# Kernel optimization log

Hardware: AMD Instinct MI355X
Metric: run time of the kernel (lower is better)

## Reference

```python
import jax, jax.numpy as jnp
import numpy as np

EMB = 1024
HEADS = 16
B, T = 4, 2048


def setup_inputs() -> dict:
    key = jax.random.key(0)
    ks = jax.random.split(key, 9)
    s = 1.0 / np.sqrt(EMB)
    return {
        "x": jax.random.normal(ks[0], (B, T, EMB), dtype=jnp.float32),
        "Wq": jax.random.normal(ks[1], (EMB, EMB), dtype=jnp.float32) * s,
        "bq": jnp.zeros((EMB,), dtype=jnp.float32),
        "Wk": jax.random.normal(ks[2], (EMB, EMB), dtype=jnp.float32) * s,
        "bk": jnp.zeros((EMB,), dtype=jnp.float32),
        "Wv": jax.random.normal(ks[3], (EMB, EMB), dtype=jnp.float32) * s,
        "bv": jnp.zeros((EMB,), dtype=jnp.float32),
        "Wo": jax.random.normal(ks[4], (EMB, EMB), dtype=jnp.float32) * s,
        "bo": jnp.zeros((EMB,), dtype=jnp.float32),
    }


def reference(x, Wq, bq, Wk, bk, Wv, bv, Wo, bo):
    b, t, e = x.shape
    h = HEADS
    hd = e // h
    scale = 1.0 / np.sqrt(hd).astype(np.float32)

    q = (x @ Wq + bq).reshape(b, t, h, hd).transpose(0, 2, 1, 3)  # [b,h,t,hd]
    k = (x @ Wk + bk).reshape(b, t, h, hd).transpose(0, 2, 1, 3)
    v = (x @ Wv + bv).reshape(b, t, h, hd).transpose(0, 2, 1, 3)

    scores = jnp.einsum('bhqd,bhkd->bhqk', q, k) * scale  # [b,h,t,t]
    causal = jnp.tril(jnp.ones((t, t), dtype=bool))  # strict upper triangle masked
    scores = jnp.where(causal, scores, -jnp.inf)
    attn = jax.nn.softmax(scores, axis=-1)
    out = jnp.einsum('bhqk,bhkd->bhqd', attn, v)  # [b,h,t,hd]
    out = out.transpose(0, 2, 1, 3).reshape(b, t, e)
    return out @ Wo + bo
```

## Files before the change

kernel.cpp:

```cpp
#include <hip/hip_runtime.h>
#include <hip/hip_bf16.h>

#define TT   2048
#define NB   4
#define EMB_ 1024
#define NH   16
#define HD   64

typedef __bf16 bf16x8 __attribute__((ext_vector_type(8)));
typedef float  f32x4  __attribute__((ext_vector_type(4)));
typedef short  short4v __attribute__((ext_vector_type(4)));

__device__ inline short f2bf(float f) {
  unsigned u = __builtin_bit_cast(unsigned, f);
  u += 0x7fffu + ((u >> 16) & 1u);
  return (short)(u >> 16);
}

__device__ __forceinline__ unsigned pk2bf(float a, float b) {
  unsigned ua = __builtin_bit_cast(unsigned, a);
  unsigned ub = __builtin_bit_cast(unsigned, b);
  ua += 0x7fffu + ((ua >> 16) & 1u);
  ub += 0x7fffu + ((ub >> 16) & 1u);
  return __builtin_amdgcn_perm(ub, ua, 0x07060302u);
}

__device__ __forceinline__ void gl_lds16(const short* g, short* l) {
  __builtin_amdgcn_global_load_lds(
      (const __attribute__((address_space(1))) unsigned int*)g,
      (__attribute__((address_space(3))) unsigned int*)l, 16, 0, 0);
}

__global__ void convert_w(const float* __restrict__ Wq, const float* __restrict__ Wk,
                          const float* __restrict__ Wv, const float* __restrict__ Wo,
                          short* __restrict__ Wt) {
  __shared__ short tile[32][33];
  const float* W = (blockIdx.z == 0) ? Wq : (blockIdx.z == 1) ? Wk
                   : (blockIdx.z == 2) ? Wv : Wo;
  short* out = Wt + (size_t)blockIdx.z * EMB_ * EMB_;
  int k0 = blockIdx.x * 32, n0 = blockIdx.y * 32;
  int t = threadIdx.x;
  int r = t >> 3, c4 = (t & 7) * 4;
  f32x4 v = *(const f32x4*)&W[(size_t)(k0 + r) * EMB_ + n0 + c4];
#pragma unroll
  for (int j = 0; j < 4; j++) tile[r][c4 + j] = f2bf(v[j]);
  __syncthreads();
  short4v w;
#pragma unroll
  for (int j = 0; j < 4; j++) w[j] = tile[c4 + j][r];
  *(short4v*)&out[(size_t)(n0 + r) * EMB_ + k0 + c4] = w;
}

__global__ void convert_x(const float* __restrict__ x, short* __restrict__ xb) {
  size_t i = ((size_t)blockIdx.x * 256 + threadIdx.x) * 8;
  f32x4 a = *(const f32x4*)&x[i];
  f32x4 b = *(const f32x4*)&x[i + 4];
  short t[8];
#pragma unroll
  for (int j = 0; j < 4; j++) { t[j] = f2bf(a[j]); t[4 + j] = f2bf(b[j]); }
  *(bf16x8*)&xb[i] = *(const bf16x8*)t;
}

__global__ __launch_bounds__(512, 2)
void gemm8(const short* __restrict__ A, const short* __restrict__ W,
           const float* __restrict__ b0, const float* __restrict__ b1,
           const float* __restrict__ b2,
           void* O0, void* O1, void* O2, int vmode_z, int o32, int scale_z) {
  __shared__ __align__(16) short S[65536];
  const int tid = threadIdx.x;
  const int wave = tid >> 6, lane = tid & 63;
  const int lg = lane >> 4, lc = lane & 15;
  const int wm = (wave >> 2) * 128, wn = (wave & 3) * 64;
  const int m0 = blockIdx.x * 256;
  const int n0g = blockIdx.y * 256;
  const int z = n0g >> 10;
  const float* bias = (z == 0) ? b0 : (z == 1) ? b1 : b2;
  void* Out = (z == 0) ? O0 : (z == 1) ? O1 : O2;
  const bool vmode = (z == vmode_z);
  const float osc = (z == scale_z) ? 0.125f : 1.0f;

  const int srow = lane >> 3;
  const int scol = ((lane & 7) ^ srow) * 8;
  const int g0 = ((0 * 4 + lg) ^ (lc & 7)) * 8;
  const int g1 = ((1 * 4 + lg) ^ (lc & 7)) * 8;

  f32x4 acc[8][4];
#pragma unroll
  for (int i = 0; i < 8; i++)
#pragma unroll
    for (int j = 0; j < 4; j++) acc[i][j] = (f32x4)0.0f;

  auto stA = [&](int buf, int half, int kt) {
    const int kk = kt * 64;
#pragma unroll
    for (int c = 0; c < 2; c++) {
      const int rl = half * 128 + c * 64 + wave * 8;
      gl_lds16(&A[(size_t)(m0 + rl + srow) * EMB_ + kk + scol],
               S + buf * 16384 + rl * 64);
    }
  };
  auto stB = [&](int buf, int half, int kt) {
    const int kk = kt * 64;
#pragma unroll
    for (int c = 0; c < 2; c++) {
      const int rl = half * 128 + c * 64 + wave * 8;
      gl_lds16(&W[(size_t)(n0g + rl + srow) * EMB_ + kk + scol],
               S + 32768 + buf * 16384 + rl * 64);
    }
  };

  stA(0, 0, 0); stA(0, 1, 0); stB(0, 0, 0); stB(0, 1, 0);
  stA(1, 0, 1); stA(1, 1, 1); stB(1, 0, 1); stB(1, 1, 1);
  asm volatile("s_waitcnt vmcnt(8)" ::: "memory");
  __builtin_amdgcn_sched_barrier(0);
  __builtin_amdgcn_s_barrier();

  const int NT = EMB_ / 64;
  bf16x8 af[4][2], bN01[2][2], bN23[2][2];

#pragma unroll 1
  for (int kt = 0; kt < NT; kt++) {
    const int cur = kt & 1, nxt = cur ^ 1;
    const short* Ac = S + cur * 16384;
    const short* Bc = S + 32768 + cur * 16384;

#pragma unroll
    for (int mi = 0; mi < 4; mi++) {
      af[mi][0] = *(const bf16x8*)&Ac[(wm + mi * 16 + lc) * 64 + g0];
      af[mi][1] = *(const bf16x8*)&Ac[(wm + mi * 16 + lc) * 64 + g1];
    }
#pragma unroll
    for (int ni = 0; ni < 2; ni++) {
      bN01[ni][0] = *(const bf16x8*)&Bc[(wn + ni * 16 + lc) * 64 + g0];
      bN01[ni][1] = *(const bf16x8*)&Bc[(wn + ni * 16 + lc) * 64 + g1];
    }
    if (kt > 0 && kt + 1 < NT) stA(nxt, 0, kt + 1);
    __builtin_amdgcn_s_barrier();
    asm volatile("s_waitcnt lgkmcnt(0)" ::: "memory");
    __builtin_amdgcn_sched_barrier(0);
    __builtin_amdgcn_s_setprio(1);
#pragma unroll
    for (int mi = 0; mi < 4; mi++)
#pragma unroll
      for (int ni = 0; ni < 2; ni++) {
        acc[mi][ni] = __builtin_amdgcn_mfma_f32_16x16x32_bf16(af[mi][0], bN01[ni][0], acc[mi][ni], 0, 0, 0);
        acc[mi][ni] = __builtin_amdgcn_mfma_f32_16x16x32_bf16(af[mi][1], bN01[ni][1], acc[mi][ni], 0, 0, 0);
      }
    __builtin_amdgcn_s_setprio(0);
    __builtin_amdgcn_s_barrier();

#pragma unroll
    for (int ni = 0; ni < 2; ni++) {
      bN23[ni][0] = *(const bf16x8*)&Bc[(wn + (ni + 2) * 16 + lc) * 64 + g0];
      bN23[ni][1] = *(const bf16x8*)&Bc[(wn + (ni + 2) * 16 + lc) * 64 + g1];
    }
    if (kt > 0 && kt + 1 < NT) stA(nxt, 1, kt + 1);
    __builtin_amdgcn_s_barrier();
    asm volatile("s_waitcnt lgkmcnt(0)" ::: "memory");
    __builtin_amdgcn_sched_barrier(0);
    __builtin_amdgcn_s_setprio(1);
#pragma unroll
    for (int mi = 0; mi < 4; mi++)
#pragma unroll
      for (int ni = 0; ni < 2; ni++) {
        acc[mi][ni + 2] = __builtin_amdgcn_mfma_f32_16x16x32_bf16(af[mi][0], bN23[ni][0], acc[mi][ni + 2], 0, 0, 0);
        acc[mi][ni + 2] = __builtin_amdgcn_mfma_f32_16x16x32_bf16(af[mi][1], bN23[ni][1], acc[mi][ni + 2], 0, 0, 0);
      }
    __builtin_amdgcn_s_setprio(0);
    __builtin_amdgcn_s_barrier();

#pragma unroll
    for (int mi = 0; mi < 4; mi++) {
      af[mi][0] = *(const bf16x8*)&Ac[(wm + (mi + 4) * 16 + lc) * 64 + g0];
      af[mi][1] = *(const bf16x8*)&Ac[(wm + (mi + 4) * 16 + lc) * 64 + g1];
    }
    if (kt + 2 < NT) stB(cur, 0, kt + 2);
    __builtin_amdgcn_s_barrier();
    asm volatile("s_waitcnt lgkmcnt(0)" ::: "memory");
    __builtin_amdgcn_sched_barrier(0);
    __builtin_amdgcn_s_setprio(1);
#pragma unroll
    for (int mi = 0; mi < 4; mi++)
#pragma unroll
      for (int ni = 0; ni < 2; ni++) {
        acc[mi + 4][ni] = __builtin_amdgcn_mfma_f32_16x16x32_bf16(af[mi][0], bN01[ni][0], acc[mi + 4][ni], 0, 0, 0);
        acc[mi + 4][ni] = __builtin_amdgcn_mfma_f32_16x16x32_bf16(af[mi][1], bN01[ni][1], acc[mi + 4][ni], 0, 0, 0);
      }
    __builtin_amdgcn_s_setprio(0);
    __builtin_amdgcn_s_barrier();

    if (kt + 2 < NT) stB(cur, 1, kt + 2);
    __builtin_amdgcn_s_barrier();
    __builtin_amdgcn_s_setprio(1);
#pragma unroll
    for (int mi = 0; mi < 4; mi++)
#pragma unroll
      for (int ni = 0; ni < 2; ni++) {
        acc[mi + 4][ni + 2] = __builtin_amdgcn_mfma_f32_16x16x32_bf16(af[mi][0], bN23[ni][0], acc[mi + 4][ni + 2], 0, 0, 0);
        acc[mi + 4][ni + 2] = __builtin_amdgcn_mfma_f32_16x16x32_bf16(af[mi][1], bN23[ni][1], acc[mi + 4][ni + 2], 0, 0, 0);
      }
    __builtin_amdgcn_s_setprio(0);
    if (kt == NT - 2) {
      asm volatile("s_waitcnt vmcnt(0)" ::: "memory");
    } else if (kt < NT - 2) {
      asm volatile("s_waitcnt vmcnt(4)" ::: "memory");
    }
    __builtin_amdgcn_sched_barrier(0);
    __builtin_amdgcn_s_barrier();
  }

#pragma unroll
  for (int ni = 0; ni < 4; ni++) {
    int colg = n0g + wn + ni * 16 + lc;
    int col = colg & (EMB_ - 1);
    float bv = bias[col];
#pragma unroll
    for (int mi = 0; mi < 8; mi++) {
#pragma unroll
      for (int r = 0; r < 4; r++) {
        int row = m0 + wm + mi * 16 + lg * 4 + r;
        float v = (acc[mi][ni][r] + bv) * osc;
        if (vmode) {
          int b = row >> 11, t = row & (TT - 1);
          int h = col >> 6, d = col & (HD - 1);
          ((short*)Out)[((size_t)((b * NH + h) * HD + d)) * TT + t] = f2bf(v);
        } else if (o32) {
          ((float*)Out)[(size_t)row * EMB_ + col] = v;
        } else {
          ((short*)Out)[(size_t)row * EMB_ + col] = f2bf(v);
        }
      }
    }
  }
}

__global__ __launch_bounds__(256, 4)
void gemm_bt(const void* __restrict__ A, int a32,
             const short* __restrict__ WtBase,
             const float* __restrict__ b0, const float* __restrict__ b1,
             const float* __restrict__ b2,
             void* O0, void* O1, void* O2, int vmode_z, int o32, int scale_z) {
  __shared__ __align__(16) short As[128 * 72];
  __shared__ __align__(16) short Bs[128 * 72];
  const int tid = threadIdx.x;
  const int z = blockIdx.z;
  const short* W    = WtBase + (size_t)z * EMB_ * EMB_;
  const float* bias = (z == 0) ? b0 : (z == 1) ? b1 : b2;
  void* Out         = (z == 0) ? O0 : (z == 1) ? O1 : O2;
  const bool vmode = (z == vmode_z);
  const float osc = (z == scale_z) ? 0.125f : 1.0f;

  const int m0 = blockIdx.x * 128;
  const int n0 = blockIdx.y * 128;
  const int wave = tid >> 6, lane = tid & 63;
  const int wm = (wave >> 1) * 64, wn = (wave & 1) * 64;
  const int lg = lane >> 4, lc = lane & 15;

  f32x4 acc[4][4];
#pragma unroll
  for (int i = 0; i < 4; i++)
#pragma unroll
    for (int j = 0; j < 4; j++) acc[i][j] = (f32x4)0.0f;

  for (int kk = 0; kk < EMB_; kk += 64) {
    __syncthreads();
#pragma unroll
    for (int i = 0; i < 4; i++) {
      int s = i * 256 + tid;
      int row = s >> 3, c = s & 7;
      size_t base = (size_t)(m0 + row) * EMB_ + kk + c * 8;
      bf16x8 av;
      if (a32) {
        const float* Af = (const float*)A + base;
        f32x4 u0 = *(const f32x4*)Af;
        f32x4 u1 = *(const f32x4*)(Af + 4);
        short tmp[8];
#pragma unroll
        for (int j = 0; j < 4; j++) { tmp[j] = f2bf(u0[j]); tmp[4 + j] = f2bf(u1[j]); }
        av = *(const bf16x8*)tmp;
      } else {
        av = *(const bf16x8*)((const short*)A + base);
      }
      *(bf16x8*)&As[row * 72 + c * 8] = av;
    }
#pragma unroll
    for (int i = 0; i < 4; i++) {
      int s = i * 256 + tid;
      int row = s >> 3, c = s & 7;
      *(bf16x8*)&Bs[row * 72 + c * 8] =
          *(const bf16x8*)&W[(size_t)(n0 + row) * EMB_ + kk + c * 8];
    }
    __syncthreads();
#pragma unroll
    for (int ks = 0; ks < 2; ks++) {
      bf16x8 af[4], bfr[4];
#pragma unroll
      for (int mi = 0; mi < 4; mi++)
        af[mi] = *(const bf16x8*)&As[(wm + mi * 16 + lc) * 72 + ks * 32 + lg * 8];
#pragma unroll
      for (int ni = 0; ni < 4; ni++)
        bfr[ni] = *(const bf16x8*)&Bs[(wn + ni * 16 + lc) * 72 + ks * 32 + lg * 8];
#pragma unroll
      for (int mi = 0; mi < 4; mi++)
#pragma unroll
        for (int ni = 0; ni < 4; ni++)
          acc[mi][ni] = __builtin_amdgcn_mfma_f32_16x16x32_bf16(af[mi], bfr[ni], acc[mi][ni], 0, 0, 0);
    }
  }

#pragma unroll
  for (int ni = 0; ni < 4; ni++) {
    int col = n0 + wn + ni * 16 + lc;
    float bv = bias[col];
#pragma unroll
    for (int mi = 0; mi < 4; mi++) {
#pragma unroll
      for (int r = 0; r < 4; r++) {
        int row = m0 + wm + mi * 16 + lg * 4 + r;
        float v = (acc[mi][ni][r] + bv) * osc;
        if (vmode) {
          int b = row >> 11, t = row & (TT - 1);
          int h = col >> 6, d = col & (HD - 1);
          ((short*)Out)[((size_t)((b * NH + h) * HD + d)) * TT + t] = f2bf(v);
        } else if (o32) {
          ((float*)Out)[(size_t)row * EMB_ + col] = v;
        } else {
          ((short*)Out)[(size_t)row * EMB_ + col] = f2bf(v);
        }
      }
    }
  }
}

__global__ __launch_bounds__(256, 2)
void attn_fwd(const short* Q, const short* K, const short* Vt, short* O) {
  __shared__ __align__(16) short Ks[128 * 72];
  __shared__ __align__(16) short Vs[64 * 136];
  __shared__ __align__(16) short Ps[4][16 * 72];
  const int tid = threadIdx.x;
  const int bh = blockIdx.y;
  const int b = bh >> 4, h = bh & (NH - 1);
  const int qtA = 15 - (int)blockIdx.x;
  const int qtB = (int)blockIdx.x;
  const int wave = tid >> 6, lane = tid & 63;
  const int lg = lane >> 4, lc = lane & 15;

  bf16x8 qf[2][2][2];
#pragma unroll
  for (int pt = 0; pt < 2; pt++) {
    const int qt = pt ? qtB : qtA;
#pragma unroll
    for (int rb = 0; rb < 2; rb++) {
      const int qrow = b * TT + qt * 128 + rb * 64 + wave * 16 + lc;
      qf[pt][rb][0] = *(const bf16x8*)&Q[(size_t)qrow * EMB_ + h * HD + lg * 8];
      qf[pt][rb][1] = *(const bf16x8*)&Q[(size_t)qrow * EMB_ + h * HD + 32 + lg * 8];
    }
  }

  f32x4 o[2][2][4];
#pragma unroll
  for (int pt = 0; pt < 2; pt++)
#pragma unroll
    for (int rb = 0; rb < 2; rb++)
#pragma unroll
      for (int ni = 0; ni < 4; ni++) o[pt][rb][ni] = (f32x4)0.0f;
  float lsum[2][2] = {{0.f, 0.f}, {0.f, 0.f}};

  bf16x8 kreg[4], vreg[4];

  auto issue_loads = [&](int ktt) {
    const int kb = ktt * 128;
#pragma unroll
    for (int i = 0; i < 4; i++) {
      int s = i * 256 + tid;
      kreg[i] = *(const bf16x8*)&K[(size_t)(b * TT + kb + (s >> 3)) * EMB_ + h * HD + (s & 7) * 8];
      vreg[i] = *(const bf16x8*)&Vt[(size_t)(bh * HD + (s >> 4)) * TT + kb + (s & 15) * 8];
    }
  };
  auto write_lds = [&]() {
#pragma unroll
    for (int i = 0; i < 4; i++) {
      int s = i * 256 + tid;
      *(bf16x8*)&Ks[(s >> 3) * 72 + (s & 7) * 8] = kreg[i];
      *(bf16x8*)&Vs[(s >> 4) * 136 + (s & 15) * 8] = vreg[i];
    }
  };

  auto compute_tile = [&](int qt, bf16x8 (&qft)[2][2], f32x4 (&ot)[2][4],
                          float (&ls)[2], int ktt) {
    const int q0 = qt * 128;
#pragma unroll
    for (int chunk = 0; chunk < 2; chunk++) {
      const int cg = 2 * ktt + chunk;
#pragma unroll
      for (int rb = 0; rb < 2; rb++) {
        const int qbase = q0 + rb * 64 + wave * 16;
        if (cg * 64 > qbase + 15) continue;
        const bool diag = (cg == 2 * qt + rb);
        const int qg = qbase + lc;

        f32x4 s4[4];
#pragma unroll
        for (int ni = 0; ni < 4; ni++) s4[ni] = (f32x4)0.0f;
#pragma unroll
        for (int ks = 0; ks < 2; ks++) {
          bf16x8 kf[4];
#pragma unroll
          for (int ni = 0; ni < 4; ni++)
            kf[ni] = *(const bf16x8*)&Ks[(chunk * 64 + ni * 16 + lc) * 72 + ks * 32 + lg * 8];
#pragma unroll
          for (int ni = 0; ni < 4; ni++)
            s4[ni] = __builtin_amdgcn_mfma_f32_16x16x32_bf16(kf[ni], qft[rb][ks], s4[ni], 0, 0, 0);
        }

#pragma unroll
        for (int ni = 0; ni < 4; ni++) {
          float p[4];
#pragma unroll
          for (int r = 0; r < 4; r++) {
            float v = s4[ni][r];
            if (diag) {
              int keyg = cg * 64 + ni * 16 + lg * 4 + r;
              if (keyg > qg) v = -1e30f;
            }
            p[r] = __expf(v - 6.0f);
            ls[rb] += p[r];
          }
          uint2 dd;
          dd.x = pk2bf(p[0], p[1]);
          dd.y = pk2bf(p[2], p[3]);
          *(uint2*)&Ps[wave][lc * 72 + ni * 16 + lg * 4] = dd;
        }

#pragma unroll
        for (int ks2 = 0; ks2 < 2; ks2++) {
          bf16x8 pa = *(const bf16x8*)&Ps[wave][lc * 72 + ks2 * 32 + lg * 8];
          bf16x8 vf[4];
#pragma unroll
          for (int ni = 0; ni < 4; ni++)
            vf[ni] = *(const bf16x8*)&Vs[(ni * 16 + lc) * 136 + chunk * 64 + ks2 * 32 + lg * 8];
#pragma unroll
          for (int ni = 0; ni < 4; ni++)
            ot[rb][ni] = __builtin_amdgcn_mfma_f32_16x16x32_bf16(pa, vf[ni], ot[rb][ni], 0, 0, 0);
        }
      }
    }
  };

  const int ntiles = qtA + 1;

  issue_loads(0);
  for (int ktt = 0; ktt < ntiles; ktt++) {
    __syncthreads();
    write_lds();
    if (ktt + 1 < ntiles) issue_loads(ktt + 1);
    __syncthreads();

    compute_tile(qtA, qf[0], o[0], lsum[0], ktt);
    if (ktt <= qtB)
      compute_tile(qtB, qf[1], o[1], lsum[1], ktt);
  }

#pragma unroll
  for (int pt = 0; pt < 2; pt++) {
    const int qt = pt ? qtB : qtA;
    const int q0 = qt * 128;
    float linv[2][4];
#pragma unroll
    for (int rb = 0; rb < 2; rb++) {
      float red = lsum[pt][rb];
      red += __shfl_xor(red, 16, 64);
      red += __shfl_xor(red, 32, 64);
#pragma unroll
      for (int r = 0; r < 4; r++)
        linv[rb][r] = 1.0f / __shfl(red, lg * 4 + r, 64);
    }
#pragma unroll
    for (int rb = 0; rb < 2; rb++) {
#pragma unroll
      for (int ni = 0; ni < 4; ni++) {
#pragma unroll
        for (int r = 0; r < 4; r++) {
          int token = b * TT + q0 + rb * 64 + wave * 16 + lg * 4 + r;
          int col = h * HD + ni * 16 + lc;
          O[(size_t)token * EMB_ + col] = f2bf(o[pt][rb][ni][r] * linv[rb][r]);
        }
      }
    }
  }
}

extern "C" void kernel_launch(void* const* d_in, const int* in_sizes, int n_in,
                              void* d_out, int out_size, void* d_ws, size_t ws_size,
                              hipStream_t stream) {
  const float* x  = (const float*)d_in[0];
  const float* Wq = (const float*)d_in[1];
  const float* bq = (const float*)d_in[2];
  const float* Wk = (const float*)d_in[3];
  const float* bk = (const float*)d_in[4];
  const float* Wv = (const float*)d_in[5];
  const float* bv = (const float*)d_in[6];
  const float* Wo = (const float*)d_in[7];
  const float* bo = (const float*)d_in[8];

  short* Wt = (short*)d_ws;
  short* Qb = Wt + (size_t)4 * EMB_ * EMB_;

  convert_w<<<dim3(32, 32, 4), 256, 0, stream>>>(Wq, Wk, Wv, Wo, Wt);

  if (ws_size >= (size_t)40 * 1024 * 1024) {
    short* xb16 = Qb + (size_t)NB * TT * EMB_;
    short* Kb   = (short*)d_out;
    short* Vtb  = Kb + (size_t)NB * TT * EMB_;
    convert_x<<<dim3(4096), 256, 0, stream>>>(x, xb16);
    gemm8<<<dim3(32, 12), 512, 0, stream>>>(
        xb16, Wt, bq, bk, bv, Qb, Kb, Vtb, 2, 0, 0);
    attn_fwd<<<dim3(8, 64), 256, 0, stream>>>(Qb, Kb, Vtb, Qb);
    gemm8<<<dim3(32, 4), 512, 0, stream>>>(
        Qb, Wt + (size_t)3 * EMB_ * EMB_, bo, bo, bo,
        d_out, d_out, d_out, -1, 1, -1);
  } else if (ws_size >= (size_t)24 * 1024 * 1024) {
    short* Kb  = (short*)d_out;
    short* Vtb = Kb + (size_t)NB * TT * EMB_;
    gemm_bt<<<dim3(64, 8, 3), 256, 0, stream>>>(
        x, 1, Wt, bq, bk, bv, Qb, Kb, Vtb, 2, 0, 0);
    attn_fwd<<<dim3(8, 64), 256, 0, stream>>>(Qb, Kb, Vtb, Qb);
    gemm_bt<<<dim3(64, 8, 1), 256, 0, stream>>>(
        Qb, 0, Wt + (size_t)3 * EMB_ * EMB_, bo, bo, bo,
        d_out, d_out, d_out, -1, 1, -1);
  } else {
    for (int b = 0; b < NB; b++) {
      const float* xb = x + (size_t)b * TT * EMB_;
      float* outb = (float*)d_out + (size_t)b * TT * EMB_;
      short* Kb  = (short*)outb;
      short* Vtb = Kb + (size_t)TT * EMB_;
      gemm_bt<<<dim3(16, 8, 3), 256, 0, stream>>>(
          xb, 1, Wt, bq, bk, bv, Qb, Kb, Vtb, 2, 0, 0);
      attn_fwd<<<dim3(8, 16), 256, 0, stream>>>(Qb, Kb, Vtb, Qb);
      gemm_bt<<<dim3(16, 8, 1), 256, 0, stream>>>(
          Qb, 0, Wt + (size_t)3 * EMB_ * EMB_, bo, bo, bo,
          outb, outb, outb, -1, 1, -1);
    }
  }
}
```

Baseline: 317.2 us.

## Remap GEMM blocks across XCDs and add narrow-N output projection kernel

The QKV GEMM now uses a 1D grid with a block-index remap that places neighbouring M/N tiles on the same XCD, aiming for better L2 reuse of A and W tiles. The output projection moves to a new gemm8n kernel with 256x128 tiles, launching 256 workgroups instead of 128 so the CUs are better filled. The remap hardcodes the grid shapes (384 and 256 blocks), and the smaller N tile lowers arithmetic intensity per block.

```diff
diff --git a/kernel.cpp b/kernel.cpp
--- a/kernel.cpp
+++ b/kernel.cpp
@@ -71,8 +71,13 @@
   const int wave = tid >> 6, lane = tid & 63;
   const int lg = lane >> 4, lc = lane & 15;
   const int wm = (wave >> 2) * 128, wn = (wave & 3) * 64;
-  const int m0 = blockIdx.x * 256;
-  const int n0g = blockIdx.y * 256;
+
+  const int wg = blockIdx.x;
+  const int xcd = wg & 7, i = wg >> 3;
+  const int bm = (xcd & 3) * 8 + (i & 7);
+  const int bn = (xcd >> 2) * 6 + (i >> 3);
+  const int m0 = bm * 256;
+  const int n0g = bn * 256;
   const int z = n0g >> 10;
   const float* bias = (z == 0) ? b0 : (z == 1) ? b1 : b2;
   void* Out = (z == 0) ? O0 : (z == 1) ? O1 : O2;
@@ -86,9 +91,9 @@
 
   f32x4 acc[8][4];
 #pragma unroll
-  for (int i = 0; i < 8; i++)
-#pragma unroll
-    for (int j = 0; j < 4; j++) acc[i][j] = (f32x4)0.0f;
+  for (int a = 0; a < 8; a++)
+#pragma unroll
+    for (int j = 0; j < 4; j++) acc[a][j] = (f32x4)0.0f;
 
   auto stA = [&](int buf, int half, int kt) {
     const int kk = kt * 64;
@@ -115,11 +120,11 @@
   __builtin_amdgcn_sched_barrier(0);
   __builtin_amdgcn_s_barrier();
 
-  const int NT = EMB_ / 64;
+  const int NKT = EMB_ / 64;
   bf16x8 af[4][2], bN01[2][2], bN23[2][2];
 
 #pragma unroll 1
-  for (int kt = 0; kt < NT; kt++) {
+  for (int kt = 0; kt < NKT; kt++) {
     const int cur = kt & 1, nxt = cur ^ 1;
     const short* Ac = S + cur * 16384;
     const short* Bc = S + 32768 + cur * 16384;
@@ -134,7 +139,7 @@
       bN01[ni][0] = *(const bf16x8*)&Bc[(wn + ni * 16 + lc) * 64 + g0];
       bN01[ni][1] = *(const bf16x8*)&Bc[(wn + ni * 16 + lc) * 64 + g1];
     }
-    if (kt > 0 && kt + 1 < NT) stA(nxt, 0, kt + 1);
+    if (kt > 0 && kt + 1 < NKT) stA(nxt, 0, kt + 1);
     __builtin_amdgcn_s_barrier();
     asm volatile("s_waitcnt lgkmcnt(0)" ::: "memory");
     __builtin_amdgcn_sched_barrier(0);
@@ -154,7 +159,7 @@
       bN23[ni][0] = *(const bf16x8*)&Bc[(wn + (ni + 2) * 16 + lc) * 64 + g0];
       bN23[ni][1] = *(const bf16x8*)&Bc[(wn + (ni + 2) * 16 + lc) * 64 + g1];
     }
-    if (kt > 0 && kt + 1 < NT) stA(nxt, 1, kt + 1);
+    if (kt > 0 && kt + 1 < NKT) stA(nxt, 1, kt + 1);
     __builtin_amdgcn_s_barrier();
     asm volatile("s_waitcnt lgkmcnt(0)" ::: "memory");
     __builtin_amdgcn_sched_barrier(0);
@@ -174,7 +179,7 @@
       af[mi][0] = *(const bf16x8*)&Ac[(wm + (mi + 4) * 16 + lc) * 64 + g0];
       af[mi][1] = *(const bf16x8*)&Ac[(wm + (mi + 4) * 16 + lc) * 64 + g1];
     }
-    if (kt + 2 < NT) stB(cur, 0, kt + 2);
+    if (kt + 2 < NKT) stB(cur, 0, kt + 2);
     __builtin_amdgcn_s_barrier();
     asm volatile("s_waitcnt lgkmcnt(0)" ::: "memory");
     __builtin_amdgcn_sched_barrier(0);
@@ -189,7 +194,7 @@
     __builtin_amdgcn_s_setprio(0);
     __builtin_amdgcn_s_barrier();
 
-    if (kt + 2 < NT) stB(cur, 1, kt + 2);
+    if (kt + 2 < NKT) stB(cur, 1, kt + 2);
     __builtin_amdgcn_s_barrier();
     __builtin_amdgcn_s_setprio(1);
 #pragma unroll
@@ -200,9 +205,9 @@
         acc[mi + 4][ni + 2] = __builtin_amdgcn_mfma_f32_16x16x32_bf16(af[mi][1], bN23[ni][1], acc[mi + 4][ni + 2], 0, 0, 0);
       }
     __builtin_amdgcn_s_setprio(0);
-    if (kt == NT - 2) {
+    if (kt == NKT - 2) {
       asm volatile("s_waitcnt vmcnt(0)" ::: "memory");
-    } else if (kt < NT - 2) {
+    } else if (kt < NKT - 2) {
       asm volatile("s_waitcnt vmcnt(4)" ::: "memory");
     }
     __builtin_amdgcn_sched_barrier(0);
@@ -229,6 +234,135 @@
         } else {
           ((short*)Out)[(size_t)row * EMB_ + col] = f2bf(v);
         }
+      }
+    }
+  }
+}
+
+__global__ __launch_bounds__(512, 2)
+void gemm8n(const short* __restrict__ A, const short* __restrict__ W,
+            const float* __restrict__ bias, float* __restrict__ Out) {
+  __shared__ __align__(16) short S[49152];
+  const int tid = threadIdx.x;
+  const int wave = tid >> 6, lane = tid & 63;
+  const int lg = lane >> 4, lc = lane & 15;
+  const int wm = (wave >> 2) * 128, wn = (wave & 3) * 32;
+
+  const int wg = blockIdx.x;
+  const int xcd = wg & 7, i = wg >> 3;
+  const int bm = (xcd & 3) * 8 + (i & 7);
+  const int bn = (xcd >> 2) * 4 + (i >> 3);
+  const int m0 = bm * 256;
+  const int n0 = bn * 128;
+
+  const int srow = lane >> 3;
+  const int scol = ((lane & 7) ^ srow) * 8;
+  const int g0 = ((0 * 4 + lg) ^ (lc & 7)) * 8;
+  const int g1 = ((1 * 4 + lg) ^ (lc & 7)) * 8;
+
+  f32x4 acc[8][2];
+#pragma unroll
+  for (int a = 0; a < 8; a++)
+#pragma unroll
+    for (int j = 0; j < 2; j++) acc[a][j] = (f32x4)0.0f;
+
+  auto stA = [&](int buf, int half, int kt) {
+    const int kk = kt * 64;
+#pragma unroll
+    for (int c = 0; c < 2; c++) {
+      const int rl = half * 128 + c * 64 + wave * 8;
+      gl_lds16(&A[(size_t)(m0 + rl + srow) * EMB_ + kk + scol],
+               S + buf * 16384 + rl * 64);
+    }
+  };
+  auto stB = [&](int buf, int kt) {
+    const int kk = kt * 64;
+#pragma unroll
+    for (int c = 0; c < 2; c++) {
+      const int rl = c * 64 + wave * 8;
+      gl_lds16(&W[(size_t)(n0 + rl + srow) * EMB_ + kk + scol],
+               S + 32768 + buf * 8192 + rl * 64);
+    }
+  };
+
+  stA(0, 0, 0); stA(0, 1, 0); stB(0, 0);
+  stA(1, 0, 1); stA(1, 1, 1); stB(1, 1);
+  asm volatile("s_waitcnt vmcnt(6)" ::: "memory");
+  __builtin_amdgcn_sched_barrier(0);
+  __builtin_amdgcn_s_barrier();
+
+  const int NKT = EMB_ / 64;
+  bf16x8 af[4][2], bN[2][2];
+
+#pragma unroll 1
+  for (int kt = 0; kt < NKT; kt++) {
+    const int cur = kt & 1, nxt = cur ^ 1;
+    const short* Ac = S + cur * 16384;
+    const short* Bc = S + 32768 + cur * 8192;
+
+#pragma unroll
+    for (int mi = 0; mi < 4; mi++) {
+      af[mi][0] = *(const bf16x8*)&Ac[(wm + mi * 16 + lc) * 64 + g0];
+      af[mi][1] = *(const bf16x8*)&Ac[(wm + mi * 16 + lc) * 64 + g1];
+    }
+#pragma unroll
+    for (int ni = 0; ni < 2; ni++) {
+      bN[ni][0] = *(const bf16x8*)&Bc[(wn + ni * 16 + lc) * 64 + g0];
+      bN[ni][1] = *(const bf16x8*)&Bc[(wn + ni * 16 + lc) * 64 + g1];
+    }
+    if (kt > 0 && kt + 1 < NKT) stA(nxt, 0, kt + 1);
+    __builtin_amdgcn_s_barrier();
+    asm volatile("s_waitcnt lgkmcnt(0)" ::: "memory");
+    __builtin_amdgcn_sched_barrier(0);
+    __builtin_amdgcn_s_setprio(1);
+#pragma unroll
+    for (int mi = 0; mi < 4; mi++)
+#pragma unroll
+      for (int ni = 0; ni < 2; ni++) {
+        acc[mi][ni] = __builtin_amdgcn_mfma_f32_16x16x32_bf16(af[mi][0], bN[ni][0], acc[mi][ni], 0, 0, 0);
+        acc[mi][ni] = __builtin_amdgcn_mfma_f32_16x16x32_bf16(af[mi][1], bN[ni][1], acc[mi][ni], 0, 0, 0);
+      }
+    __builtin_amdgcn_s_setprio(0);
+    __builtin_amdgcn_s_barrier();
+
+#pragma unroll
+    for (int mi = 0; mi < 4; mi++) {
+      af[mi][0] = *(const bf16x8*)&Ac[(wm + (mi + 4) * 16 + lc) * 64 + g0];
+      af[mi][1] = *(const bf16x8*)&Ac[(wm + (mi + 4) * 16 + lc) * 64 + g1];
+    }
+    if (kt > 0 && kt + 1 < NKT) stA(nxt, 1, kt + 1);
+    if (kt + 2 < NKT) stB(cur, kt + 2);
+    __builtin_amdgcn_s_barrier();
+    asm volatile("s_waitcnt lgkmcnt(0)" ::: "memory");
+    __builtin_amdgcn_sched_barrier(0);
+    __builtin_amdgcn_s_setprio(1);
+#pragma unroll
+    for (int mi = 0; mi < 4; mi++)
+#pragma unroll
+      for (int ni = 0; ni < 2; ni++) {
+        acc[mi + 4][ni] = __builtin_amdgcn_mfma_f32_16x16x32_bf16(af[mi][0], bN[ni][0], acc[mi + 4][ni], 0, 0, 0);
+        acc[mi + 4][ni] = __builtin_amdgcn_mfma_f32_16x16x32_bf16(af[mi][1], bN[ni][1], acc[mi + 4][ni], 0, 0, 0);
+      }
+    __builtin_amdgcn_s_setprio(0);
+    if (kt == NKT - 2) {
+      asm volatile("s_waitcnt vmcnt(0)" ::: "memory");
+    } else if (kt < NKT - 2) {
+      asm volatile("s_waitcnt vmcnt(2)" ::: "memory");
+    }
+    __builtin_amdgcn_sched_barrier(0);
+    __builtin_amdgcn_s_barrier();
+  }
+
+#pragma unroll
+  for (int ni = 0; ni < 2; ni++) {
+    int col = n0 + wn + ni * 16 + lc;
+    float bv = bias[col];
+#pragma unroll
+    for (int mi = 0; mi < 8; mi++) {
+#pragma unroll
+      for (int r = 0; r < 4; r++) {
+        int row = m0 + wm + mi * 16 + lg * 4 + r;
+        Out[(size_t)row * EMB_ + col] = acc[mi][ni][r] + bv;
       }
     }
   }
@@ -513,12 +647,11 @@
     short* Kb   = (short*)d_out;
     short* Vtb  = Kb + (size_t)NB * TT * EMB_;
     convert_x<<<dim3(4096), 256, 0, stream>>>(x, xb16);
-    gemm8<<<dim3(32, 12), 512, 0, stream>>>(
+    gemm8<<<dim3(384), 512, 0, stream>>>(
         xb16, Wt, bq, bk, bv, Qb, Kb, Vtb, 2, 0, 0);
     attn_fwd<<<dim3(8, 64), 256, 0, stream>>>(Qb, Kb, Vtb, Qb);
-    gemm8<<<dim3(32, 4), 512, 0, stream>>>(
-        Qb, Wt + (size_t)3 * EMB_ * EMB_, bo, bo, bo,
-        d_out, d_out, d_out, -1, 1, -1);
+    gemm8n<<<dim3(256), 512, 0, stream>>>(
+        Qb, Wt + (size_t)3 * EMB_ * EMB_, bo, (float*)d_out);
   } else if (ws_size >= (size_t)24 * 1024 * 1024) {
     short* Kb  = (short*)d_out;
     short* Vtb = Kb + (size_t)NB * TT * EMB_;
```

After: 300.4 us. 5.3% less time.
